# Optimization experiments

Measured on AMD Instinct MI355X. Metric: run time of the kernel, lower is better.

The kernel has to match this reference:

```python
import jax, jax.numpy as jnp
import numpy as np

HIDDEN_DIM = 2048
N = 4  # expansion_rate
LAYER_IDX = 0
S_ALPHA = 0.01
S_BETA = 0.01
EPS = 1e-5


def setup_inputs() -> dict:
    key = jax.random.key(0)
    k1, k2, k3, k4, k5 = jax.random.split(key, 5)
    batch, seq = 4, 2048
    layer_output = jax.random.normal(k1, (batch, seq, HIDDEN_DIM), dtype=jnp.float32)
    hidden_states = jax.random.normal(k2, (batch, seq, N, HIDDEN_DIM), dtype=jnp.float32)
    # static base matrices (initialization from the torch module)
    B = jnp.ones((1, N), dtype=jnp.float32)
    Am = jnp.zeros((N, 1), dtype=jnp.float32).at[LAYER_IDX % N, 0].set(1.0)
    Ar = jnp.eye(N, dtype=jnp.float32)
    # dynamic parameters
    s_alpha = jnp.full((N, N), S_ALPHA, dtype=jnp.float32)
    s_beta = jnp.full((1, N), S_BETA, dtype=jnp.float32)
    W_beta = jax.random.normal(k3, (HIDDEN_DIM, N), dtype=jnp.float32) * 0.02
    W_m = jax.random.normal(k4, (HIDDEN_DIM, N), dtype=jnp.float32) * 0.02
    W_r = jax.random.normal(k5, (HIDDEN_DIM, N, N), dtype=jnp.float32) * 0.02
    return {
        "layer_output": layer_output,
        "hidden_states": hidden_states,
        "B": B,
        "Am": Am,
        "Ar": Ar,
        "s_alpha": s_alpha,
        "s_beta": s_beta,
        "W_beta": W_beta,
        "W_m": W_m,
        "W_r": W_r,
    }


def reference(layer_output, hidden_states, B, Am, Ar, s_alpha, s_beta, W_beta, W_m, W_r):
    # hidden_states: [b, s, n, d]; layer_output: [b, s, d]
    # --- dynamic matrices ---
    mu = jnp.mean(hidden_states, axis=-1, keepdims=True)
    var = jnp.var(hidden_states, axis=-1, keepdims=True)
    H_norm = (hidden_states - mu) * jax.lax.rsqrt(var + EPS)  # layer_norm, no affine
    H_bar = H_norm.mean(axis=2)  # [b, s, d]

    delta_B = jnp.tanh(H_bar @ W_beta)            # [b, s, n]
    B_dyn = s_beta[0] * delta_B + B[0]            # [b, s, n]
    delta_Am = jnp.tanh(H_bar @ W_m)              # [b, s, n]
    Am_dyn = s_alpha[:, 0] * delta_Am + Am[:, 0]  # [b, s, n]
    delta_Ar = jnp.tanh(jnp.einsum('bsd,dij->bsij', H_bar, W_r))  # [b, s, n, n]
    Ar_dyn = s_alpha * delta_Ar + Ar              # [b, s, n, n]

    # --- combine ---
    depth = B_dyn[..., None] * layer_output[:, :, None, :]                       # [b,s,n,d]
    mixed = jnp.einsum('bsn,bsnd->bsd', Am_dyn, hidden_states)[:, :, None, :]    # [b,s,1,d] broadcasts over n
    residual = jnp.einsum('bsij,bsjd->bsid', Ar_dyn, hidden_states)              # [b,s,n,d]
    return depth + mixed + residual
```

## Files before the change

### kernel.cpp

```cpp
#include <hip/hip_runtime.h>

#define D     2048
#define NEXP  4
#define BLK   256
#define NWAVE 4
#define EPSV  1e-5f

__global__ __launch_bounds__(256) void wt_kernel(
    const float* __restrict__ Wb, const float* __restrict__ Wm,
    const float* __restrict__ Wr, float* __restrict__ Wt)
{
    int idx = blockIdx.x * 256 + threadIdx.x;
    int c = idx / D;
    int d = idx % D;
    float v;
    if (c < 4)       v = Wb[d * 4 + c];
    else if (c < 8)  v = Wm[d * 4 + (c - 4)];
    else             v = Wr[d * 16 + (c - 8)];
    Wt[c * D + d] = v;
}

__global__ __launch_bounds__(BLK) void hc_kernel(
    const float* __restrict__ lo,
    const float* __restrict__ hs,
    const float* __restrict__ Bm,
    const float* __restrict__ Am,
    const float* __restrict__ Ar,
    const float* __restrict__ s_alpha,
    const float* __restrict__ s_beta,
    const float* __restrict__ Wt,
    float* __restrict__ out)
{
    __shared__ float hb_lds[D];
    __shared__ float red[NWAVE][2 * NEXP];
    __shared__ float stats[2][NEXP];
    __shared__ float coef[24];

    const int tid  = threadIdx.x;
    const int wave = tid >> 6;
    const int lane = tid & 63;
    const long tok = blockIdx.x;

    const float4* hs4  = (const float4*)(hs + tok * (long)(NEXP * D));
    const float4* lo4  = (const float4*)(lo + tok * (long)D);
    float4*       out4 = (float4*)(out + tok * (long)(NEXP * D));

    float4 h[NEXP][2];
    float sum[NEXP], sq[NEXP];
    #pragma unroll
    for (int n = 0; n < NEXP; ++n) { sum[n] = 0.f; sq[n] = 0.f; }

    #pragma unroll
    for (int n = 0; n < NEXP; ++n) {
        #pragma unroll
        for (int k = 0; k < 2; ++k) {
            float4 v = hs4[n * (D / 4) + tid + BLK * k];
            h[n][k] = v;
            sum[n] += v.x + v.y + v.z + v.w;
            sq[n]  += v.x * v.x + v.y * v.y + v.z * v.z + v.w * v.w;
        }
    }
    float4 lpre0 = lo4[tid];
    float4 lpre1 = lo4[tid + BLK];

    #pragma unroll
    for (int n = 0; n < NEXP; ++n) {
        #pragma unroll
        for (int off = 32; off > 0; off >>= 1) {
            sum[n] += __shfl_xor(sum[n], off, 64);
            sq[n]  += __shfl_xor(sq[n],  off, 64);
        }
    }
    if (lane == 0) {
        #pragma unroll
        for (int n = 0; n < NEXP; ++n) {
            red[wave][n]        = sum[n];
            red[wave][NEXP + n] = sq[n];
        }
    }
    __syncthreads();
    if (tid < NEXP) {
        float s = 0.f, s2 = 0.f;
        #pragma unroll
        for (int w = 0; w < NWAVE; ++w) { s += red[w][tid]; s2 += red[w][NEXP + tid]; }
        float m   = s * (1.f / D);
        float var = s2 * (1.f / D) - m * m;
        stats[0][tid] = m;
        stats[1][tid] = rsqrtf(var + EPSV);
    }
    __syncthreads();
    float mu[NEXP], rs[NEXP];
    #pragma unroll
    for (int n = 0; n < NEXP; ++n) { mu[n] = stats[0][n]; rs[n] = stats[1][n]; }

    #pragma unroll
    for (int k = 0; k < 2; ++k) {
        int d4 = tid + BLK * k;
        float4 hb;
        hb.x = 0.25f * ((h[0][k].x - mu[0]) * rs[0] + (h[1][k].x - mu[1]) * rs[1] +
                        (h[2][k].x - mu[2]) * rs[2] + (h[3][k].x - mu[3]) * rs[3]);
        hb.y = 0.25f * ((h[0][k].y - mu[0]) * rs[0] + (h[1][k].y - mu[1]) * rs[1] +
                        (h[2][k].y - mu[2]) * rs[2] + (h[3][k].y - mu[3]) * rs[3]);
        hb.z = 0.25f * ((h[0][k].z - mu[0]) * rs[0] + (h[1][k].z - mu[1]) * rs[1] +
                        (h[2][k].z - mu[2]) * rs[2] + (h[3][k].z - mu[3]) * rs[3]);
        hb.w = 0.25f * ((h[0][k].w - mu[0]) * rs[0] + (h[1][k].w - mu[1]) * rs[1] +
                        (h[2][k].w - mu[2]) * rs[2] + (h[3][k].w - mu[3]) * rs[3]);
        ((float4*)hb_lds)[d4] = hb;
    }
    __syncthreads();

    float acc[6];
    #pragma unroll
    for (int c = 0; c < 6; ++c) acc[c] = 0.f;

    const int cbase = wave * 6;
    const float4* Wt4 = (const float4*)Wt;

    #pragma unroll
    for (int p = 0; p < 8; ++p) {
        int d4 = p * 64 + lane;
        float4 hb = ((const float4*)hb_lds)[d4];
        #pragma unroll
        for (int c = 0; c < 6; ++c) {
            float4 w = Wt4[(cbase + c) * (D / 4) + d4];
            acc[c] += hb.x * w.x + hb.y * w.y + hb.z * w.z + hb.w * w.w;
        }
    }
    #pragma unroll
    for (int c = 0; c < 6; ++c) {
        #pragma unroll
        for (int off = 32; off > 0; off >>= 1)
            acc[c] += __shfl_xor(acc[c], off, 64);
    }
    if (lane == 0) {
        #pragma unroll
        for (int c = 0; c < 6; ++c) coef[cbase + c] = acc[c];
    }
    __syncthreads();
    if (tid < 24) {
        float t = tanhf(coef[tid]);
        float c;
        if (tid < 4) {
            c = s_beta[tid] * t + Bm[tid];
        } else if (tid < 8) {
            int n = tid - 4;
            c = s_alpha[n * 4] * t + Am[n];
        } else {
            int ij = tid - 8;
            c = s_alpha[ij] * t + Ar[ij];
        }
        coef[tid] = c;
    }
    __syncthreads();

    float Bd[NEXP], Amd[NEXP], Ard[NEXP][NEXP];
    #pragma unroll
    for (int n = 0; n < NEXP; ++n) { Bd[n] = coef[n]; Amd[n] = coef[4 + n]; }
    #pragma unroll
    for (int i = 0; i < NEXP; ++i)
        #pragma unroll
        for (int j = 0; j < NEXP; ++j) Ard[i][j] = coef[8 + i * 4 + j];

    #pragma unroll
    for (int k = 0; k < 2; ++k) {
        int d4 = tid + BLK * k;
        float4 l = (k == 0) ? lpre0 : lpre1;

        float4 mx = {0.f, 0.f, 0.f, 0.f};
        #pragma unroll
        for (int n = 0; n < NEXP; ++n) {
            mx.x += Amd[n] * h[n][k].x; mx.y += Amd[n] * h[n][k].y;
            mx.z += Amd[n] * h[n][k].z; mx.w += Amd[n] * h[n][k].w;
        }
        #pragma unroll
        for (int i = 0; i < NEXP; ++i) {
            float4 o;
            o.x = Bd[i] * l.x + mx.x;
            o.y = Bd[i] * l.y + mx.y;
            o.z = Bd[i] * l.z + mx.z;
            o.w = Bd[i] * l.w + mx.w;
            #pragma unroll
            for (int j = 0; j < NEXP; ++j) {
                o.x += Ard[i][j] * h[j][k].x;
                o.y += Ard[i][j] * h[j][k].y;
                o.z += Ard[i][j] * h[j][k].z;
                o.w += Ard[i][j] * h[j][k].w;
            }
            out4[i * (D / 4) + d4] = o;
        }
    }
}

extern "C" void kernel_launch(void* const* d_in, const int* in_sizes, int n_in,
                              void* d_out, int out_size, void* d_ws, size_t ws_size,
                              hipStream_t stream) {
    const float* lo      = (const float*)d_in[0];
    const float* hs      = (const float*)d_in[1];
    const float* Bm      = (const float*)d_in[2];
    const float* Am      = (const float*)d_in[3];
    const float* Ar      = (const float*)d_in[4];
    const float* s_alpha = (const float*)d_in[5];
    const float* s_beta  = (const float*)d_in[6];
    const float* Wb      = (const float*)d_in[7];
    const float* Wm      = (const float*)d_in[8];
    const float* Wr      = (const float*)d_in[9];
    float* out = (float*)d_out;
    float* Wt  = (float*)d_ws;

    wt_kernel<<<192, 256, 0, stream>>>(Wb, Wm, Wr, Wt);

    const int tokens = in_sizes[0] / D;
    hc_kernel<<<tokens, BLK, 0, stream>>>(lo, hs, Bm, Am, Ar, s_alpha, s_beta,
                                          Wt, out);
}
```

Measured before the change: 157.2 us.

## Process two tokens per block and stash hidden states as bf16 in LDS

Each block now handles two tokens, so every weight load from Wt is reused for both tokens' projections. Hidden states are packed to bf16 in shared memory instead of kept in fp32 registers, and normalization is recomputed on the fly during the dot product. This halves weight traffic per token and frees registers. The price is lower precision: the final output is computed from the bf16-rounded hidden states, which can fail a tight fp32 tolerance.

```diff
diff --git a/kernel.cpp b/kernel.cpp
--- a/kernel.cpp
+++ b/kernel.cpp
@@ -4,7 +4,20 @@
 #define NEXP  4
 #define BLK   256
 #define NWAVE 4
+#define NTOK  2
 #define EPSV  1e-5f
+
+__device__ __forceinline__ float bl(unsigned int u) {
+    union { unsigned int x; float f; } v; v.x = u << 16; return v.f;
+}
+__device__ __forceinline__ float bh(unsigned int u) {
+    union { unsigned int x; float f; } v; v.x = u & 0xffff0000u; return v.f;
+}
+__device__ __forceinline__ unsigned int pk2(float x, float y) {
+    unsigned int r;
+    asm volatile("v_cvt_pk_bf16_f32 %0, %1, %2" : "=v"(r) : "v"(x), "v"(y));
+    return r;
+}
 
 __global__ __launch_bounds__(256) void wt_kernel(
     const float* __restrict__ Wb, const float* __restrict__ Wm,
@@ -31,87 +44,101 @@
     const float* __restrict__ Wt,
     float* __restrict__ out)
 {
-    __shared__ float hb_lds[D];
-    __shared__ float red[NWAVE][2 * NEXP];
-    __shared__ float stats[2][NEXP];
-    __shared__ float coef[24];
+    __shared__ unsigned int h16[NTOK][NEXP][D / 2];
+    __shared__ float red[NWAVE][NTOK * 2 * NEXP];
+    __shared__ float stats[NTOK][2][NEXP];
+    __shared__ float coef[NTOK][24];
 
     const int tid  = threadIdx.x;
     const int wave = tid >> 6;
     const int lane = tid & 63;
-    const long tok = blockIdx.x;
-
-    const float4* hs4  = (const float4*)(hs + tok * (long)(NEXP * D));
-    const float4* lo4  = (const float4*)(lo + tok * (long)D);
-    float4*       out4 = (float4*)(out + tok * (long)(NEXP * D));
-
-    float4 h[NEXP][2];
-    float sum[NEXP], sq[NEXP];
-    #pragma unroll
-    for (int n = 0; n < NEXP; ++n) { sum[n] = 0.f; sq[n] = 0.f; }
-
-    #pragma unroll
-    for (int n = 0; n < NEXP; ++n) {
-        #pragma unroll
-        for (int k = 0; k < 2; ++k) {
-            float4 v = hs4[n * (D / 4) + tid + BLK * k];
-            h[n][k] = v;
-            sum[n] += v.x + v.y + v.z + v.w;
-            sq[n]  += v.x * v.x + v.y * v.y + v.z * v.z + v.w * v.w;
-        }
-    }
-    float4 lpre0 = lo4[tid];
-    float4 lpre1 = lo4[tid + BLK];
-
-    #pragma unroll
-    for (int n = 0; n < NEXP; ++n) {
-        #pragma unroll
-        for (int off = 32; off > 0; off >>= 1) {
-            sum[n] += __shfl_xor(sum[n], off, 64);
-            sq[n]  += __shfl_xor(sq[n],  off, 64);
-        }
-    }
+    const long tok0 = (long)blockIdx.x * NTOK;
+
+    const float4* hs4[NTOK];
+    const float4* lo4[NTOK];
+    float4*       out4[NTOK];
+    #pragma unroll
+    for (int t = 0; t < NTOK; ++t) {
+        hs4[t]  = (const float4*)(hs + (tok0 + t) * (long)(NEXP * D));
+        lo4[t]  = (const float4*)(lo + (tok0 + t) * (long)D);
+        out4[t] = (float4*)(out + (tok0 + t) * (long)(NEXP * D));
+    }
+
+    float sum[NTOK][NEXP], sq[NTOK][NEXP];
+    #pragma unroll
+    for (int t = 0; t < NTOK; ++t)
+        #pragma unroll
+        for (int n = 0; n < NEXP; ++n) { sum[t][n] = 0.f; sq[t][n] = 0.f; }
+
+    #pragma unroll
+    for (int t = 0; t < NTOK; ++t) {
+        #pragma unroll
+        for (int n = 0; n < NEXP; ++n) {
+            #pragma unroll
+            for (int k = 0; k < 2; ++k) {
+                int d4 = tid + BLK * k;
+                float4 v = hs4[t][n * (D / 4) + d4];
+                sum[t][n] += v.x + v.y + v.z + v.w;
+                sq[t][n]  += v.x * v.x + v.y * v.y + v.z * v.z + v.w * v.w;
+                uint2 p;
+                p.x = pk2(v.x, v.y);
+                p.y = pk2(v.z, v.w);
+                ((uint2*)h16[t][n])[d4] = p;
+            }
+        }
+    }
+    float4 lpre[NTOK][2];
+    #pragma unroll
+    for (int t = 0; t < NTOK; ++t) {
+        lpre[t][0] = lo4[t][tid];
+        lpre[t][1] = lo4[t][tid + BLK];
+    }
+
+    #pragma unroll
+    for (int t = 0; t < NTOK; ++t)
+        #pragma unroll
+        for (int n = 0; n < NEXP; ++n) {
+            #pragma unroll
+            for (int off = 32; off > 0; off >>= 1) {
+                sum[t][n] += __shfl_xor(sum[t][n], off, 64);
+                sq[t][n]  += __shfl_xor(sq[t][n],  off, 64);
+            }
+        }
     if (lane == 0) {
         #pragma unroll
-        for (int n = 0; n < NEXP; ++n) {
-            red[wave][n]        = sum[n];
-            red[wave][NEXP + n] = sq[n];
-        }
-    }
-    __syncthreads();
-    if (tid < NEXP) {
+        for (int t = 0; t < NTOK; ++t)
+            #pragma unroll
+            for (int n = 0; n < NEXP; ++n) {
+                red[wave][t * 8 + n]        = sum[t][n];
+                red[wave][t * 8 + NEXP + n] = sq[t][n];
+            }
+    }
+    __syncthreads();
+    if (tid < NTOK * NEXP) {
+        int t = tid >> 2, n = tid & 3;
         float s = 0.f, s2 = 0.f;
         #pragma unroll
-        for (int w = 0; w < NWAVE; ++w) { s += red[w][tid]; s2 += red[w][NEXP + tid]; }
+        for (int w = 0; w < NWAVE; ++w) {
+            s  += red[w][t * 8 + n];
+            s2 += red[w][t * 8 + NEXP + n];
+        }
         float m   = s * (1.f / D);
         float var = s2 * (1.f / D) - m * m;
-        stats[0][tid] = m;
-        stats[1][tid] = rsqrtf(var + EPSV);
-    }
-    __syncthreads();
-    float mu[NEXP], rs[NEXP];
-    #pragma unroll
-    for (int n = 0; n < NEXP; ++n) { mu[n] = stats[0][n]; rs[n] = stats[1][n]; }
-
-    #pragma unroll
-    for (int k = 0; k < 2; ++k) {
-        int d4 = tid + BLK * k;
-        float4 hb;
-        hb.x = 0.25f * ((h[0][k].x - mu[0]) * rs[0] + (h[1][k].x - mu[1]) * rs[1] +
-                        (h[2][k].x - mu[2]) * rs[2] + (h[3][k].x - mu[3]) * rs[3]);
-        hb.y = 0.25f * ((h[0][k].y - mu[0]) * rs[0] + (h[1][k].y - mu[1]) * rs[1] +
-                        (h[2][k].y - mu[2]) * rs[2] + (h[3][k].y - mu[3]) * rs[3]);
-        hb.z = 0.25f * ((h[0][k].z - mu[0]) * rs[0] + (h[1][k].z - mu[1]) * rs[1] +
-                        (h[2][k].z - mu[2]) * rs[2] + (h[3][k].z - mu[3]) * rs[3]);
-        hb.w = 0.25f * ((h[0][k].w - mu[0]) * rs[0] + (h[1][k].w - mu[1]) * rs[1] +
-                        (h[2][k].w - mu[2]) * rs[2] + (h[3][k].w - mu[3]) * rs[3]);
-        ((float4*)hb_lds)[d4] = hb;
-    }
-    __syncthreads();
-
-    float acc[6];
-    #pragma unroll
-    for (int c = 0; c < 6; ++c) acc[c] = 0.f;
+        stats[t][0][n] = m;
+        stats[t][1][n] = rsqrtf(var + EPSV);
+    }
+    __syncthreads();
+    float mu[NTOK][NEXP], rs[NTOK][NEXP];
+    #pragma unroll
+    for (int t = 0; t < NTOK; ++t)
+        #pragma unroll
+        for (int n = 0; n < NEXP; ++n) { mu[t][n] = stats[t][0][n]; rs[t][n] = stats[t][1][n]; }
+
+    float acc[NTOK][6];
+    #pragma unroll
+    for (int t = 0; t < NTOK; ++t)
+        #pragma unroll
+        for (int c = 0; c < 6; ++c) acc[t][c] = 0.f;
 
     const int cbase = wave * 6;
     const float4* Wt4 = (const float4*)Wt;
@@ -119,74 +146,106 @@
     #pragma unroll
     for (int p = 0; p < 8; ++p) {
         int d4 = p * 64 + lane;
-        float4 hb = ((const float4*)hb_lds)[d4];
+        float4 hb[NTOK];
+        #pragma unroll
+        for (int t = 0; t < NTOK; ++t) {
+            uint2 r0 = ((const uint2*)h16[t][0])[d4];
+            uint2 r1 = ((const uint2*)h16[t][1])[d4];
+            uint2 r2 = ((const uint2*)h16[t][2])[d4];
+            uint2 r3 = ((const uint2*)h16[t][3])[d4];
+            hb[t].x = 0.25f * ((bl(r0.x) - mu[t][0]) * rs[t][0] + (bl(r1.x) - mu[t][1]) * rs[t][1] +
+                               (bl(r2.x) - mu[t][2]) * rs[t][2] + (bl(r3.x) - mu[t][3]) * rs[t][3]);
+            hb[t].y = 0.25f * ((bh(r0.x) - mu[t][0]) * rs[t][0] + (bh(r1.x) - mu[t][1]) * rs[t][1] +
+                               (bh(r2.x) - mu[t][2]) * rs[t][2] + (bh(r3.x) - mu[t][3]) * rs[t][3]);
+            hb[t].z = 0.25f * ((bl(r0.y) - mu[t][0]) * rs[t][0] + (bl(r1.y) - mu[t][1]) * rs[t][1] +
+                               (bl(r2.y) - mu[t][2]) * rs[t][2] + (bl(r3.y) - mu[t][3]) * rs[t][3]);
+            hb[t].w = 0.25f * ((bh(r0.y) - mu[t][0]) * rs[t][0] + (bh(r1.y) - mu[t][1]) * rs[t][1] +
+                               (bh(r2.y) - mu[t][2]) * rs[t][2] + (bh(r3.y) - mu[t][3]) * rs[t][3]);
+        }
         #pragma unroll
         for (int c = 0; c < 6; ++c) {
             float4 w = Wt4[(cbase + c) * (D / 4) + d4];
-            acc[c] += hb.x * w.x + hb.y * w.y + hb.z * w.z + hb.w * w.w;
-        }
-    }
-    #pragma unroll
-    for (int c = 0; c < 6; ++c) {
-        #pragma unroll
-        for (int off = 32; off > 0; off >>= 1)
-            acc[c] += __shfl_xor(acc[c], off, 64);
-    }
+            #pragma unroll
+            for (int t = 0; t < NTOK; ++t)
+                acc[t][c] += hb[t].x * w.x + hb[t].y * w.y + hb[t].z * w.z + hb[t].w * w.w;
+        }
+    }
+    #pragma unroll
+    for (int t = 0; t < NTOK; ++t)
+        #pragma unroll
+        for (int c = 0; c < 6; ++c) {
+            #pragma unroll
+            for (int off = 32; off > 0; off >>= 1)
+                acc[t][c] += __shfl_xor(acc[t][c], off, 64);
+        }
     if (lane == 0) {
         #pragma unroll
-        for (int c = 0; c < 6; ++c) coef[cbase + c] = acc[c];
-    }
-    __syncthreads();
-    if (tid < 24) {
-        float t = tanhf(coef[tid]);
-        float c;
-        if (tid < 4) {
-            c = s_beta[tid] * t + Bm[tid];
-        } else if (tid < 8) {
-            int n = tid - 4;
-            c = s_alpha[n * 4] * t + Am[n];
+        for (int t = 0; t < NTOK; ++t)
+            #pragma unroll
+            for (int c = 0; c < 6; ++c) coef[t][cbase + c] = acc[t][c];
+    }
+    __syncthreads();
+    if (tid < NTOK * 24) {
+        int t = tid / 24, c = tid % 24;
+        float tv = tanhf(coef[t][c]);
+        float cv;
+        if (c < 4) {
+            cv = s_beta[c] * tv + Bm[c];
+        } else if (c < 8) {
+            int n = c - 4;
+            cv = s_alpha[n * 4] * tv + Am[n];
         } else {
-            int ij = tid - 8;
-            c = s_alpha[ij] * t + Ar[ij];
-        }
-        coef[tid] = c;
-    }
-    __syncthreads();
-
-    float Bd[NEXP], Amd[NEXP], Ard[NEXP][NEXP];
-    #pragma unroll
-    for (int n = 0; n < NEXP; ++n) { Bd[n] = coef[n]; Amd[n] = coef[4 + n]; }
-    #pragma unroll
-    for (int i = 0; i < NEXP; ++i)
-        #pragma unroll
-        for (int j = 0; j < NEXP; ++j) Ard[i][j] = coef[8 + i * 4 + j];
-
-    #pragma unroll
-    for (int k = 0; k < 2; ++k) {
-        int d4 = tid + BLK * k;
-        float4 l = (k == 0) ? lpre0 : lpre1;
-
-        float4 mx = {0.f, 0.f, 0.f, 0.f};
-        #pragma unroll
-        for (int n = 0; n < NEXP; ++n) {
-            mx.x += Amd[n] * h[n][k].x; mx.y += Amd[n] * h[n][k].y;
-            mx.z += Amd[n] * h[n][k].z; mx.w += Amd[n] * h[n][k].w;
-        }
-        #pragma unroll
-        for (int i = 0; i < NEXP; ++i) {
-            float4 o;
-            o.x = Bd[i] * l.x + mx.x;
-            o.y = Bd[i] * l.y + mx.y;
-            o.z = Bd[i] * l.z + mx.z;
-            o.w = Bd[i] * l.w + mx.w;
-            #pragma unroll
-            for (int j = 0; j < NEXP; ++j) {
-                o.x += Ard[i][j] * h[j][k].x;
-                o.y += Ard[i][j] * h[j][k].y;
-                o.z += Ard[i][j] * h[j][k].z;
-                o.w += Ard[i][j] * h[j][k].w;
-            }
-            out4[i * (D / 4) + d4] = o;
+            int ij = c - 8;
+            cv = s_alpha[ij] * tv + Ar[ij];
+        }
+        coef[t][c] = cv;
+    }
+    __syncthreads();
+
+    #pragma unroll
+    for (int t = 0; t < NTOK; ++t) {
+        float Bd[NEXP], Amd[NEXP], Ard[NEXP][NEXP];
+        #pragma unroll
+        for (int n = 0; n < NEXP; ++n) { Bd[n] = coef[t][n]; Amd[n] = coef[t][4 + n]; }
+        #pragma unroll
+        for (int i = 0; i < NEXP; ++i)
+            #pragma unroll
+            for (int j = 0; j < NEXP; ++j) Ard[i][j] = coef[t][8 + i * 4 + j];
+
+        #pragma unroll
+        for (int k = 0; k < 2; ++k) {
+            int d4 = tid + BLK * k;
+            float4 h[NEXP];
+            #pragma unroll
+            for (int n = 0; n < NEXP; ++n) {
+                uint2 r = ((const uint2*)h16[t][n])[d4];
+                h[n].x = bl(r.x); h[n].y = bh(r.x);
+                h[n].z = bl(r.y); h[n].w = bh(r.y);
+            }
+            float4 l = lpre[t][k];
+
+            float4 mx = {0.f, 0.f, 0.f, 0.f};
+            #pragma unroll
+            for (int n = 0; n < NEXP; ++n) {
+                mx.x += Amd[n] * h[n].x; mx.y += Amd[n] * h[n].y;
+                mx.z += Amd[n] * h[n].z; mx.w += Amd[n] * h[n].w;
+            }
+            #pragma unroll
+            for (int i = 0; i < NEXP; ++i) {
+                float4 o;
+                o.x = Bd[i] * l.x + mx.x;
+                o.y = Bd[i] * l.y + mx.y;
+                o.z = Bd[i] * l.z + mx.z;
+                o.w = Bd[i] * l.w + mx.w;
+                #pragma unroll
+                for (int j = 0; j < NEXP; ++j) {
+                    o.x += Ard[i][j] * h[j].x;
+                    o.y += Ard[i][j] * h[j].y;
+                    o.z += Ard[i][j] * h[j].z;
+                    o.w += Ard[i][j] * h[j].w;
+                }
+                out4[t][i * (D / 4) + d4] = o;
+            }
         }
     }
 }
@@ -210,6 +269,6 @@
     wt_kernel<<<192, 256, 0, stream>>>(Wb, Wm, Wr, Wt);
 
     const int tokens = in_sizes[0] / D;
-    hc_kernel<<<tokens, BLK, 0, stream>>>(lo, hs, Bm, Am, Ar, s_alpha, s_beta,
-                                          Wt, out);
-}
+    hc_kernel<<<tokens / NTOK, BLK, 0, stream>>>(lo, hs, Bm, Am, Ar, s_alpha, s_beta,
+                                                 Wt, out);
+}
```

After: 185.0 us. +17.7%, slower.
